# Kernel tuning notes

Hardware: AMD Instinct MI355X
Metric: run time of the kernel (lower is better)

Reference implementation:

```python
import jax, jax.numpy as jnp
import numpy as np

DIM = 1024
HEADS = 16
SCALE = DIM ** (-0.5)  # note: full dim, matching original module


def setup_inputs() -> dict:
    key = jax.random.key(0)
    k1, k2, k3, k4 = jax.random.split(key, 4)
    x = jax.random.normal(k1, (8, 1024, DIM), dtype=jnp.float32)
    w_qkv = jax.random.normal(k2, (DIM, 3 * DIM), dtype=jnp.float32) * (DIM ** -0.5)
    w_out = jax.random.normal(k3, (DIM, DIM), dtype=jnp.float32) * (DIM ** -0.5)
    b_out = jax.random.normal(k4, (DIM,), dtype=jnp.float32) * 0.01
    return {"x": x, "w_qkv": w_qkv, "w_out": w_out, "b_out": b_out}


def reference(x, w_qkv, w_out, b_out):
    b, n, dim = x.shape
    h = HEADS
    d = dim // h
    qkv = x @ w_qkv  # [b, n, 3*dim]
    q, k, v = jnp.split(qkv, 3, axis=-1)
    # 'b n (h d) -> b h n d'
    def to_heads(t):
        return t.reshape(b, n, h, d).transpose(0, 2, 1, 3)
    q, k, v = to_heads(q), to_heads(k), to_heads(v)
    dots = jnp.einsum('bhid,bhjd->bhij', q, k) * SCALE
    attn = jax.nn.softmax(dots, axis=-1)
    out = jnp.einsum('bhij,bhjd->bhid', attn, v)
    out = out.transpose(0, 2, 1, 3).reshape(b, n, dim)  # 'b h n d -> b n (h d)'
    return out @ w_out + b_out  # dropout is identity (rate=0 / eval)
```

## Files before the change

### kernel.cpp

```cpp
#include <hip/hip_runtime.h>

typedef __bf16 bf16x8 __attribute__((ext_vector_type(8)));
typedef __bf16 bf16x4 __attribute__((ext_vector_type(4)));
typedef float  f32x4  __attribute__((ext_vector_type(4)));

#define MFMA16(a, b, c) __builtin_amdgcn_mfma_f32_16x16x32_bf16(a, b, c, 0, 0, 0)
#define GLL(gp, lp) __builtin_amdgcn_global_load_lds( \
    (__attribute__((address_space(1))) void*)(gp),    \
    (__attribute__((address_space(3))) void*)(lp), 16, 0, 0)
#define WAITBAR(N) asm volatile("s_waitcnt vmcnt(" #N ") lgkmcnt(0)\n\ts_barrier" ::: "memory")

__global__ __launch_bounds__(256) void cast_x_kernel(const float* __restrict__ in,
                                                     __bf16* __restrict__ out) {
  int i = blockIdx.x * 256 + threadIdx.x;
  const float4 v = ((const float4*)in)[i];
  bf16x4 o = {(__bf16)v.x, (__bf16)v.y, (__bf16)v.z, (__bf16)v.w};
  ((bf16x4*)out)[i] = o;
}

__global__ void transpose_cast_kernel(const float* __restrict__ in,
                                      __bf16* __restrict__ out,
                                      int rows, int cols) {
  __shared__ float tile[32][33];
  int tx = threadIdx.x, ty = threadIdx.y;
  int x = blockIdx.x * 32 + tx;
  int y0 = blockIdx.y * 32;
#pragma unroll
  for (int i = 0; i < 32; i += 8)
    tile[ty + i][tx] = in[(y0 + ty + i) * cols + x];
  __syncthreads();
  int ox = y0 + tx;
  int oy0 = blockIdx.x * 32;
#pragma unroll
  for (int i = 0; i < 32; i += 8)
    out[(oy0 + ty + i) * rows + ox] = (__bf16)tile[tx][ty + i];
}

#define QSCALE 0.045084220027780106f
__global__ __launch_bounds__(256) void gemm_bt_kernel(
    const __bf16* __restrict__ A, const __bf16* __restrict__ Bt, int mode, int nxg,
    __bf16* __restrict__ qo, __bf16* __restrict__ ko, __bf16* __restrict__ vo,
    float* __restrict__ outp, const float* __restrict__ bias) {
  __shared__ __bf16 LDS[3][2][4096];
  const int tid = threadIdx.x;
  const int id = blockIdx.x;
  const int xcd = id & 7, s = id >> 3;
  const int bx = xcd * nxg + (nxg == 3 ? s % 3 : 0);
  const int by = (nxg == 3 ? s / 3 : s);
  const int m0 = by * 128, n0 = bx * 128;
  const int w = tid >> 6, lane = tid & 63;
  const int quad = lane >> 4, l15 = lane & 15;
  const int wm = (w >> 1) * 64, wn = (w & 1) * 64;
  f32x4 acc[4][4] = {};
  const int sr = tid >> 2;
  const int sc = (tid & 3) * 8;
  const __bf16* ag = A + (m0 + sr) * 1024 + sc;
  const __bf16* bg = Bt + (n0 + sr) * 1024 + sc;

  auto stage = [&](int T, int b) {
    const int kk = T * 32;
    GLL(ag + kk,             &LDS[b][0][0] + w * 512);
    GLL(ag + 64 * 1024 + kk, &LDS[b][0][0] + 2048 + w * 512);
    GLL(bg + kk,             &LDS[b][1][0] + w * 512);
    GLL(bg + 64 * 1024 + kk, &LDS[b][1][0] + 2048 + w * 512);
  };
  auto compute = [&](int b) {
    const __bf16* Asb = &LDS[b][0][0];
    const __bf16* Bsb = &LDS[b][1][0];
    bf16x8 af[4], bfr[4];
#pragma unroll
    for (int i = 0; i < 4; ++i)
      af[i] = *(const bf16x8*)(Asb + (wm + i * 16 + l15) * 32 + quad * 8);
#pragma unroll
    for (int j = 0; j < 4; ++j)
      bfr[j] = *(const bf16x8*)(Bsb + (wn + j * 16 + l15) * 32 + quad * 8);
#pragma unroll
    for (int i = 0; i < 4; ++i)
#pragma unroll
      for (int j = 0; j < 4; ++j)
        acc[i][j] = MFMA16(af[i], bfr[j], acc[i][j]);
  };

  stage(0, 0);
  stage(1, 1);
  WAITBAR(4);
  for (int g = 0; g < 10; ++g) {
    const int t = g * 3;
    stage(t + 2, 2); compute(0); WAITBAR(4);
    stage(t + 3, 0); compute(1); WAITBAR(4);
    stage(t + 4, 1); compute(2); WAITBAR(4);
  }
  compute(0);
  asm volatile("s_waitcnt vmcnt(0) lgkmcnt(0)\n\ts_barrier" ::: "memory");
  compute(1);
  __syncthreads();

  const int gcw = n0 + wn;
  float* T = (float*)(&LDS[0][0][0]) + w * 1088;
  if (mode == 0) {
    const int which = gcw >> 10;
    const int h = (gcw & 1023) >> 6;
    if (which == 2) {
#pragma unroll
      for (int i = 0; i < 4; ++i) {
        int gm = m0 + wm + i * 16 + quad * 4;
        int b = gm >> 10, n = gm & 1023;
        __bf16* vb = vo + ((long)(b * 16 + h) * 64) * 1024 + n;
#pragma unroll
        for (int j = 0; j < 4; ++j) {
          int dd = j * 16 + l15;
          bf16x4 pv = {(__bf16)acc[i][j][0], (__bf16)acc[i][j][1],
                       (__bf16)acc[i][j][2], (__bf16)acc[i][j][3]};
          *(bf16x4*)(vb + (long)dd * 1024) = pv;
        }
      }
    } else {
      __bf16* dst = (which == 0) ? qo : ko;
      const float scl = (which == 0) ? QSCALE : 1.0f;
#pragma unroll
      for (int i = 0; i < 4; ++i) {
#pragma unroll
        for (int j = 0; j < 4; ++j)
#pragma unroll
          for (int r = 0; r < 4; ++r)
            T[(quad * 4 + r) * 68 + j * 16 + l15] = acc[i][j][r];
        const float* Tr = T + l15 * 68 + quad * 16;
        f32x4 c0 = *(const f32x4*)(Tr);
        f32x4 c1 = *(const f32x4*)(Tr + 4);
        f32x4 c2 = *(const f32x4*)(Tr + 8);
        f32x4 c3 = *(const f32x4*)(Tr + 12);
        int gm = m0 + wm + i * 16 + l15;
        int b = gm >> 10, n = gm & 1023;
        __bf16* p = dst + ((long)((b * 16 + h) * 1024 + n)) * 64 + quad * 16;
        bf16x8 o0 = {(__bf16)(c0[0] * scl), (__bf16)(c0[1] * scl),
                     (__bf16)(c0[2] * scl), (__bf16)(c0[3] * scl),
                     (__bf16)(c1[0] * scl), (__bf16)(c1[1] * scl),
                     (__bf16)(c1[2] * scl), (__bf16)(c1[3] * scl)};
        bf16x8 o1 = {(__bf16)(c2[0] * scl), (__bf16)(c2[1] * scl),
                     (__bf16)(c2[2] * scl), (__bf16)(c2[3] * scl),
                     (__bf16)(c3[0] * scl), (__bf16)(c3[1] * scl),
                     (__bf16)(c3[2] * scl), (__bf16)(c3[3] * scl)};
        *(bf16x8*)p = o0;
        *(bf16x8*)(p + 8) = o1;
      }
    }
  } else {
    const int cb = gcw;
    f32x4 bv[4];
#pragma unroll
    for (int c = 0; c < 4; ++c)
      bv[c] = *(const f32x4*)(bias + cb + quad * 16 + c * 4);
#pragma unroll
    for (int i = 0; i < 4; ++i) {
#pragma unroll
      for (int j = 0; j < 4; ++j)
#pragma unroll
        for (int r = 0; r < 4; ++r)
          T[(quad * 4 + r) * 68 + j * 16 + l15] = acc[i][j][r];
      const float* Tr = T + l15 * 68 + quad * 16;
      int gm = m0 + wm + i * 16 + l15;
      float* p = outp + (long)gm * 1024 + cb + quad * 16;
#pragma unroll
      for (int c = 0; c < 4; ++c) {
        f32x4 v = *(const f32x4*)(Tr + c * 4);
        v += bv[c];
        *(f32x4*)(p + c * 4) = v;
      }
    }
  }
}

__global__ __launch_bounds__(256, 4) void attn_kernel(
    const __bf16* __restrict__ q, const __bf16* __restrict__ k,
    const __bf16* __restrict__ vt, __bf16* __restrict__ ao) {
  __shared__ __bf16 KV[2][128 * 64];
  __shared__ __bf16 Ps[4][32 * 32];
  __bf16* const Ks = KV[0];
  __bf16* const Vs = KV[1];
  const int tid = threadIdx.x;
  const int bh = blockIdx.x & 127, qt = blockIdx.x >> 7;
  const int w = tid >> 6, lane = tid & 63;
  const int quad = lane >> 4, l15 = lane & 15;
  const int qrow = qt * 128 + w * 32;
  const __bf16* qb = q + (bh * 1024 + qrow) * 64;
  bf16x8 qf[2][2];
#pragma unroll
  for (int f = 0; f < 2; ++f) {
    qf[f][0] = *(const bf16x8*)(qb + (f * 16 + l15) * 64 + quad * 8);
    qf[f][1] = *(const bf16x8*)(qb + (f * 16 + l15) * 64 + 32 + quad * 8);
  }
  f32x4 o[2][4] = {};
  float rs0 = 0.f, rs1 = 0.f;
  const int krow = tid >> 3, kg8 = tid & 7;
  const __bf16* kg = k + (bh * 1024 + krow) * 64 + kg8 * 8;
  const int ksw = (kg8 ^ (krow & 7)) * 8;
  const int vrow = tid >> 2, vg4 = tid & 3;
  const __bf16* vg = vt + (bh * 64 + vrow) * 1024 + vg4 * 8;
  const int kfs0 = (quad ^ (l15 & 7)) * 8;
  const int kfs1 = ((4 + quad) ^ (l15 & 7)) * 8;
  __bf16* const pw = Ps[w];
  const int psw = quad ^ (l15 & 3);

  bf16x8 kvr[4], vvr[4];
#pragma unroll
  for (int p = 0; p < 4; ++p) kvr[p] = *(const bf16x8*)(kg + (p * 32) * 64);
#pragma unroll
  for (int p = 0; p < 4; ++p) vvr[p] = *(const bf16x8*)(vg + p * 32);

  for (int jt = 0; jt < 8; ++jt) {
    __syncthreads();
#pragma unroll
    for (int p = 0; p < 4; ++p)
      *(bf16x8*)(Ks + (krow + p * 32) * 64 + ksw) = kvr[p];
#pragma unroll
    for (int p = 0; p < 4; ++p)
      *(bf16x8*)(Vs + vrow * 128 + (((p * 4 + vg4) ^ (vrow & 15)) * 8)) = vvr[p];
    __syncthreads();
    if (jt < 7) {
      const int j0n = (jt + 1) * 128;
#pragma unroll
      for (int p = 0; p < 4; ++p) kvr[p] = *(const bf16x8*)(kg + (j0n + p * 32) * 64);
#pragma unroll
      for (int p = 0; p < 4; ++p) vvr[p] = *(const bf16x8*)(vg + j0n + p * 32);
    }
#pragma unroll
    for (int Q = 0; Q < 4; ++Q) {
#pragma unroll
      for (int tl = 0; tl < 2; ++tl) {
        const int t = 2 * Q + tl;
        const __bf16* kr = Ks + (t * 16 + l15) * 64;
        bf16x8 kf0 = *(const bf16x8*)(kr + kfs0);
        bf16x8 kf1 = *(const bf16x8*)(kr + kfs1);
        f32x4 z0 = {}, z1 = {};
        __builtin_amdgcn_s_setprio(1);
        z0 = MFMA16(kf0, qf[0][0], z0);
        z0 = MFMA16(kf1, qf[0][1], z0);
        z1 = MFMA16(kf0, qf[1][0], z1);
        z1 = MFMA16(kf1, qf[1][1], z1);
        __builtin_amdgcn_s_setprio(0);
        const float p00 = __builtin_amdgcn_exp2f(z0[0]), p01 = __builtin_amdgcn_exp2f(z0[1]);
        const float p02 = __builtin_amdgcn_exp2f(z0[2]), p03 = __builtin_amdgcn_exp2f(z0[3]);
        const float p10 = __builtin_amdgcn_exp2f(z1[0]), p11 = __builtin_amdgcn_exp2f(z1[1]);
        const float p12 = __builtin_amdgcn_exp2f(z1[2]), p13 = __builtin_amdgcn_exp2f(z1[3]);
        rs0 += (p00 + p01) + (p02 + p03);
        rs1 += (p10 + p11) + (p12 + p13);
        const int g = (2 * tl + (quad >> 1)) ^ (l15 & 3);
        bf16x4 pa = {(__bf16)p00, (__bf16)p01, (__bf16)p02, (__bf16)p03};
        bf16x4 pb = {(__bf16)p10, (__bf16)p11, (__bf16)p12, (__bf16)p13};
        *(bf16x4*)(pw + l15 * 32 + g * 8 + (quad & 1) * 4) = pa;
        *(bf16x4*)(pw + (16 + l15) * 32 + g * 8 + (quad & 1) * 4) = pb;
      }
      bf16x8 pf0 = *(const bf16x8*)(pw + l15 * 32 + psw * 8);
      bf16x8 pf1 = *(const bf16x8*)(pw + (16 + l15) * 32 + psw * 8);
      __builtin_amdgcn_s_setprio(1);
#pragma unroll
      for (int dt = 0; dt < 4; ++dt) {
        bf16x8 vf = *(const bf16x8*)(Vs + (dt * 16 + l15) * 128 + (((Q * 4 + quad) ^ l15) * 8));
        o[0][dt] = MFMA16(pf0, vf, o[0][dt]);
        o[1][dt] = MFMA16(pf1, vf, o[1][dt]);
      }
      __builtin_amdgcn_s_setprio(0);
    }
  }
  rs0 += __shfl_xor(rs0, 16); rs0 += __shfl_xor(rs0, 32);
  rs1 += __shfl_xor(rs1, 16); rs1 += __shfl_xor(rs1, 32);
  __syncthreads();
  float* const T = (float*)KV + w * 1088;
  const int b = bh >> 4, h = bh & 15;
  const int rr = lane >> 3, c8 = lane & 7;
#pragma unroll
  for (int f = 0; f < 2; ++f) {
    const float rsf = f ? rs1 : rs0;
#pragma unroll
    for (int dt = 0; dt < 4; ++dt)
#pragma unroll
      for (int r = 0; r < 4; ++r)
        T[(quad * 4 + r) * 68 + dt * 16 + l15] = o[f][dt][r];
#pragma unroll
    for (int h2 = 0; h2 < 2; ++h2) {
      const int row = h2 * 8 + rr;
      const float inv = 1.0f / __shfl(rsf, row);
      const float* Tr = T + row * 68 + c8 * 8;
      const f32x4 a0 = *(const f32x4*)(Tr);
      const f32x4 a1 = *(const f32x4*)(Tr + 4);
      bf16x8 ov = {(__bf16)(a0[0] * inv), (__bf16)(a0[1] * inv),
                   (__bf16)(a0[2] * inv), (__bf16)(a0[3] * inv),
                   (__bf16)(a1[0] * inv), (__bf16)(a1[1] * inv),
                   (__bf16)(a1[2] * inv), (__bf16)(a1[3] * inv)};
      const long grow = (long)b * 1024 + qrow + f * 16 + row;
      *(bf16x8*)(ao + grow * 1024 + h * 64 + c8 * 8) = ov;
    }
  }
}

extern "C" void kernel_launch(void* const* d_in, const int* in_sizes, int n_in,
                              void* d_out, int out_size, void* d_ws, size_t ws_size,
                              hipStream_t stream) {
  const float* x = (const float*)d_in[0];
  const float* w_qkv = (const float*)d_in[1];
  const float* w_out = (const float*)d_in[2];
  const float* b_out = (const float*)d_in[3];
  float* out = (float*)d_out;

  char* ws = (char*)d_ws;
  __bf16* xb    = (__bf16*)(ws);
  __bf16* wqkvt = (__bf16*)(ws + 16777216);
  __bf16* woutt = (__bf16*)(ws + 23068672);
  __bf16* qw    = (__bf16*)(ws + 25165824);
  __bf16* kw    = (__bf16*)(ws + 41943040);
  __bf16* vw    = (__bf16*)(ws + 58720256);
  __bf16* ao    = xb;

  cast_x_kernel<<<8192, 256, 0, stream>>>(x, xb);
  transpose_cast_kernel<<<dim3(96, 32), dim3(32, 8), 0, stream>>>(w_qkv, wqkvt, 1024, 3072);
  transpose_cast_kernel<<<dim3(32, 32), dim3(32, 8), 0, stream>>>(w_out, woutt, 1024, 1024);
  gemm_bt_kernel<<<1536, 256, 0, stream>>>(xb, wqkvt, 0, 3, qw, kw, vw, nullptr, nullptr);
  attn_kernel<<<1024, 256, 0, stream>>>(qw, kw, vw, ao);
  gemm_bt_kernel<<<512, 256, 0, stream>>>(ao, woutt, 1, 1, nullptr, nullptr, nullptr, out, b_out);
}
```

Before: 242.9 us.

## Replace QKV projection GEMM with 256x256-tile, 8-wave pipelined kernel

After: 245.5 us. No clear change (+1.1%).

```diff
diff --git a/kernel.cpp b/kernel.cpp
--- a/kernel.cpp
+++ b/kernel.cpp
@@ -9,6 +9,9 @@
     (__attribute__((address_space(1))) void*)(gp),    \
     (__attribute__((address_space(3))) void*)(lp), 16, 0, 0)
 #define WAITBAR(N) asm volatile("s_waitcnt vmcnt(" #N ") lgkmcnt(0)\n\ts_barrier" ::: "memory")
+#define BAR1()  asm volatile("s_barrier" ::: "memory")
+#define BAR2()  asm volatile("s_waitcnt lgkmcnt(0)\n\ts_barrier" ::: "memory")
+#define VBAR1() asm volatile("s_waitcnt vmcnt(4)\n\ts_barrier" ::: "memory")
 
 __global__ __launch_bounds__(256) void cast_x_kernel(const float* __restrict__ in,
                                                      __bf16* __restrict__ out) {
@@ -37,6 +40,156 @@
 }
 
 #define QSCALE 0.045084220027780106f
+
+__global__ __launch_bounds__(512) void gemm256_qkv(
+    const __bf16* __restrict__ A, const __bf16* __restrict__ Bt,
+    __bf16* __restrict__ qo, __bf16* __restrict__ ko, __bf16* __restrict__ vo) {
+  __shared__ __bf16 LDS[65536];
+  const int tid = threadIdx.x;
+  const int w = tid >> 6, lane = tid & 63;
+  const int quad = lane >> 4, l15 = lane & 15;
+  const int wr = w >> 2, wc = w & 3;
+  const int g = (blockIdx.x & 7) * 48 + (blockIdx.x >> 3);
+  const int by = g / 12, bx = g - by * 12;
+  const int m0 = by * 256, n0 = bx * 256;
+
+  const int srow = w * 16 + (lane >> 2);
+  const int scg = (((lane & 3) ^ (((lane >> 5) & 1) << 1))) * 8;
+  const __bf16* ag = A + (m0 + srow) * 1024 + scg;
+  const __bf16* bg = Bt + (n0 + srow) * 1024 + scg;
+
+  auto stageA = [&](int t, int h, int bufo) {
+    const __bf16* gp = ag + h * 131072 + t * 64;
+    __bf16* lp = (__bf16*)LDS + bufo + h * 8192 + w * 1024;
+    GLL(gp, lp);
+    GLL(gp + 32, lp + 512);
+  };
+  auto stageB = [&](int t, int h, int bufo) {
+    const __bf16* gp = bg + h * 131072 + t * 64;
+    __bf16* lp = (__bf16*)LDS + 32768 + bufo + h * 8192 + w * 1024;
+    GLL(gp, lp);
+    GLL(gp + 32, lp + 512);
+  };
+
+  const int swq2 = (quad * 8) ^ ((l15 >> 3) << 4);
+  const __bf16* Ard = LDS + wr * 8192 + l15 * 32 + swq2;
+  const __bf16* Brd = LDS + 32768 + (wc >> 1) * 8192 + (wc & 1) * 4096 + l15 * 32 + swq2;
+
+  f32x4 acc[8][4] = {};
+  bf16x8 a[4][2], bA[2][2], bB[2][2];
+
+  auto rdA = [&](int bufo, int i0) {
+#pragma unroll
+    for (int i = 0; i < 4; ++i)
+#pragma unroll
+      for (int ks = 0; ks < 2; ++ks)
+        a[i][ks] = *(const bf16x8*)(Ard + bufo + ((i0 + i) * 2 + ks) * 512);
+  };
+  auto rdB = [&](int bufo, int j0, bf16x8 (&bb)[2][2]) {
+#pragma unroll
+    for (int j = 0; j < 2; ++j)
+#pragma unroll
+      for (int ks = 0; ks < 2; ++ks)
+        bb[j][ks] = *(const bf16x8*)(Brd + bufo + ((j0 + j) * 2 + ks) * 512);
+  };
+  auto mm = [&](int i0, bf16x8 (&bb)[2][2], int j0) {
+    __builtin_amdgcn_s_setprio(1);
+#pragma unroll
+    for (int i = 0; i < 4; ++i)
+#pragma unroll
+      for (int j = 0; j < 2; ++j)
+#pragma unroll
+        for (int ks = 0; ks < 2; ++ks)
+          acc[i0 + i][j0 + j] = MFMA16(a[i][ks], bb[j][ks], acc[i0 + i][j0 + j]);
+    __builtin_amdgcn_s_setprio(0);
+  };
+
+  stageB(0, 0, 0); stageB(0, 1, 0);
+  stageA(0, 0, 0); stageA(0, 1, 0);
+  stageB(1, 0, 16384); stageB(1, 1, 16384);
+  VBAR1();
+
+#pragma unroll 1
+  for (int it = 0; it < 8; ++it) {
+    const int t1 = 2 * it + 1;
+    const int t2 = it < 7 ? 2 * it + 2 : 15;
+    const int t3 = it < 7 ? 2 * it + 3 : 15;
+    rdA(0, 0); rdB(0, 0, bA);
+    stageA(t1, 0, 16384);
+    BAR1(); mm(0, bA, 0); BAR2();
+    rdB(0, 2, bB);
+    stageA(t1, 1, 16384);
+    BAR1(); mm(0, bB, 2); BAR2();
+    rdA(0, 4);
+    stageB(t2, 0, 0);
+    BAR1(); mm(4, bA, 0); BAR2();
+    stageB(t2, 1, 0);
+    VBAR1(); mm(4, bB, 2); BAR2();
+    rdA(16384, 0); rdB(16384, 0, bA);
+    stageA(t2, 0, 0);
+    BAR1(); mm(0, bA, 0); BAR2();
+    rdB(16384, 2, bB);
+    stageA(t2, 1, 0);
+    BAR1(); mm(0, bB, 2); BAR2();
+    rdA(16384, 4);
+    stageB(t3, 0, 16384);
+    BAR1(); mm(4, bA, 0); BAR2();
+    stageB(t3, 1, 16384);
+    VBAR1(); mm(4, bB, 2); BAR2();
+  }
+  WAITBAR(0);
+
+  const int gcw = n0 + wc * 64;
+  const int which = gcw >> 10;
+  const int h = (gcw & 1023) >> 6;
+  const int rowb = m0 + wr * 128;
+  if (which == 2) {
+#pragma unroll
+    for (int i = 0; i < 8; ++i) {
+      int gm = rowb + i * 16 + quad * 4;
+      int b = gm >> 10, n = gm & 1023;
+      __bf16* vb = vo + ((long)(b * 16 + h) * 64) * 1024 + n;
+#pragma unroll
+      for (int j = 0; j < 4; ++j) {
+        int dd = j * 16 + l15;
+        bf16x4 pv = {(__bf16)acc[i][j][0], (__bf16)acc[i][j][1],
+                     (__bf16)acc[i][j][2], (__bf16)acc[i][j][3]};
+        *(bf16x4*)(vb + (long)dd * 1024) = pv;
+      }
+    }
+  } else {
+    __bf16* dst = (which == 0) ? qo : ko;
+    const float scl = (which == 0) ? QSCALE : 1.0f;
+    float* T = (float*)LDS + w * 1088;
+#pragma unroll
+    for (int i = 0; i < 8; ++i) {
+#pragma unroll
+      for (int j = 0; j < 4; ++j)
+#pragma unroll
+        for (int r = 0; r < 4; ++r)
+          T[(quad * 4 + r) * 68 + j * 16 + l15] = acc[i][j][r];
+      const float* Tr = T + l15 * 68 + quad * 16;
+      f32x4 c0 = *(const f32x4*)(Tr);
+      f32x4 c1 = *(const f32x4*)(Tr + 4);
+      f32x4 c2 = *(const f32x4*)(Tr + 8);
+      f32x4 c3 = *(const f32x4*)(Tr + 12);
+      int gm = rowb + i * 16 + l15;
+      int b = gm >> 10, n = gm & 1023;
+      __bf16* p = dst + ((long)((b * 16 + h) * 1024 + n)) * 64 + quad * 16;
+      bf16x8 o0 = {(__bf16)(c0[0] * scl), (__bf16)(c0[1] * scl),
+                   (__bf16)(c0[2] * scl), (__bf16)(c0[3] * scl),
+                   (__bf16)(c1[0] * scl), (__bf16)(c1[1] * scl),
+                   (__bf16)(c1[2] * scl), (__bf16)(c1[3] * scl)};
+      bf16x8 o1 = {(__bf16)(c2[0] * scl), (__bf16)(c2[1] * scl),
+                   (__bf16)(c2[2] * scl), (__bf16)(c2[3] * scl),
+                   (__bf16)(c3[0] * scl), (__bf16)(c3[1] * scl),
+                   (__bf16)(c3[2] * scl), (__bf16)(c3[3] * scl)};
+      *(bf16x8*)p = o0;
+      *(bf16x8*)(p + 8) = o1;
+    }
+  }
+}
+
 __global__ __launch_bounds__(256) void gemm_bt_kernel(
     const __bf16* __restrict__ A, const __bf16* __restrict__ Bt, int mode, int nxg,
     __bf16* __restrict__ qo, __bf16* __restrict__ ko, __bf16* __restrict__ vo,
@@ -314,7 +467,7 @@
   cast_x_kernel<<<8192, 256, 0, stream>>>(x, xb);
   transpose_cast_kernel<<<dim3(96, 32), dim3(32, 8), 0, stream>>>(w_qkv, wqkvt, 1024, 3072);
   transpose_cast_kernel<<<dim3(32, 32), dim3(32, 8), 0, stream>>>(w_out, woutt, 1024, 1024);
-  gemm_bt_kernel<<<1536, 256, 0, stream>>>(xb, wqkvt, 0, 3, qw, kw, vw, nullptr, nullptr);
+  gemm256_qkv<<<384, 512, 0, stream>>>(xb, wqkvt, qw, kw, vw);
   attn_kernel<<<1024, 256, 0, stream>>>(qw, kw, vw, ao);
   gemm_bt_kernel<<<512, 256, 0, stream>>>(ao, woutt, 1, 1, nullptr, nullptr, nullptr, out, b_out);
 }
```

## Read K and V fragments directly from global memory instead of LDS staging

Applied to the files above, without the earlier changes.

Measured after the change: 312.0 us. 1.28x slower.

```diff
diff --git a/kernel.cpp b/kernel.cpp
--- a/kernel.cpp
+++ b/kernel.cpp
@@ -173,10 +173,8 @@
 __global__ __launch_bounds__(256, 4) void attn_kernel(
     const __bf16* __restrict__ q, const __bf16* __restrict__ k,
     const __bf16* __restrict__ vt, __bf16* __restrict__ ao) {
-  __shared__ __bf16 KV[2][128 * 64];
   __shared__ __bf16 Ps[4][32 * 32];
-  __bf16* const Ks = KV[0];
-  __bf16* const Vs = KV[1];
+  __shared__ float Ts[4][16 * 68];
   const int tid = threadIdx.x;
   const int bh = blockIdx.x & 127, qt = blockIdx.x >> 7;
   const int w = tid >> 6, lane = tid & 63;
@@ -191,46 +189,20 @@
   }
   f32x4 o[2][4] = {};
   float rs0 = 0.f, rs1 = 0.f;
-  const int krow = tid >> 3, kg8 = tid & 7;
-  const __bf16* kg = k + (bh * 1024 + krow) * 64 + kg8 * 8;
-  const int ksw = (kg8 ^ (krow & 7)) * 8;
-  const int vrow = tid >> 2, vg4 = tid & 3;
-  const __bf16* vg = vt + (bh * 64 + vrow) * 1024 + vg4 * 8;
-  const int kfs0 = (quad ^ (l15 & 7)) * 8;
-  const int kfs1 = ((4 + quad) ^ (l15 & 7)) * 8;
+  const __bf16* kb = k + (bh * 1024) * 64;
+  const __bf16* vb = vt + (bh * 64) * 1024;
   __bf16* const pw = Ps[w];
   const int psw = quad ^ (l15 & 3);
 
-  bf16x8 kvr[4], vvr[4];
-#pragma unroll
-  for (int p = 0; p < 4; ++p) kvr[p] = *(const bf16x8*)(kg + (p * 32) * 64);
-#pragma unroll
-  for (int p = 0; p < 4; ++p) vvr[p] = *(const bf16x8*)(vg + p * 32);
-
-  for (int jt = 0; jt < 8; ++jt) {
-    __syncthreads();
-#pragma unroll
-    for (int p = 0; p < 4; ++p)
-      *(bf16x8*)(Ks + (krow + p * 32) * 64 + ksw) = kvr[p];
-#pragma unroll
-    for (int p = 0; p < 4; ++p)
-      *(bf16x8*)(Vs + vrow * 128 + (((p * 4 + vg4) ^ (vrow & 15)) * 8)) = vvr[p];
-    __syncthreads();
-    if (jt < 7) {
-      const int j0n = (jt + 1) * 128;
-#pragma unroll
-      for (int p = 0; p < 4; ++p) kvr[p] = *(const bf16x8*)(kg + (j0n + p * 32) * 64);
-#pragma unroll
-      for (int p = 0; p < 4; ++p) vvr[p] = *(const bf16x8*)(vg + j0n + p * 32);
-    }
+  for (int j0 = 0; j0 < 1024; j0 += 128) {
 #pragma unroll
     for (int Q = 0; Q < 4; ++Q) {
 #pragma unroll
       for (int tl = 0; tl < 2; ++tl) {
         const int t = 2 * Q + tl;
-        const __bf16* kr = Ks + (t * 16 + l15) * 64;
-        bf16x8 kf0 = *(const bf16x8*)(kr + kfs0);
-        bf16x8 kf1 = *(const bf16x8*)(kr + kfs1);
+        const __bf16* kr = kb + (j0 + t * 16 + l15) * 64;
+        bf16x8 kf0 = *(const bf16x8*)(kr + quad * 8);
+        bf16x8 kf1 = *(const bf16x8*)(kr + 32 + quad * 8);
         f32x4 z0 = {}, z1 = {};
         __builtin_amdgcn_s_setprio(1);
         z0 = MFMA16(kf0, qf[0][0], z0);
@@ -255,7 +227,7 @@
       __builtin_amdgcn_s_setprio(1);
 #pragma unroll
       for (int dt = 0; dt < 4; ++dt) {
-        bf16x8 vf = *(const bf16x8*)(Vs + (dt * 16 + l15) * 128 + (((Q * 4 + quad) ^ l15) * 8));
+        bf16x8 vf = *(const bf16x8*)(vb + (dt * 16 + l15) * 1024 + j0 + (Q * 4 + quad) * 8);
         o[0][dt] = MFMA16(pf0, vf, o[0][dt]);
         o[1][dt] = MFMA16(pf1, vf, o[1][dt]);
       }
@@ -264,8 +236,7 @@
   }
   rs0 += __shfl_xor(rs0, 16); rs0 += __shfl_xor(rs0, 32);
   rs1 += __shfl_xor(rs1, 16); rs1 += __shfl_xor(rs1, 32);
-  __syncthreads();
-  float* const T = (float*)KV + w * 1088;
+  float* const T = Ts[w];
   const int b = bh >> 4, h = bh & 15;
   const int rr = lane >> 3, c8 = lane & 7;
 #pragma unroll
```
